# Optimization experiments

Measured on AMD Instinct MI355X. Metric: run time of the kernel, lower is better.

Reference implementation:

```python
import jax, jax.numpy as jnp
import numpy as np

N = 100000          # nodes
F_IN = 500          # num_features
HID = 256           # hidden
C = 40              # out_classes
E = 2302585         # ~ N*ln(N)*ec, doubled (both directions) in spar_samp
ALPHA0 = 0.1        # att[0][0] = alpha*(1-alpha)**0


def setup_inputs() -> dict:
    key = jax.random.key(0)
    ks = jax.random.split(key, 8)
    x = jax.random.normal(ks[0], (N, F_IN), dtype=jnp.float32)
    W1 = jax.random.normal(ks[1], (F_IN, HID), dtype=jnp.float32) * (1.0 / np.sqrt(F_IN))
    b1 = jnp.zeros((HID,), dtype=jnp.float32)
    W2 = jax.random.normal(ks[2], (HID, C), dtype=jnp.float32) * (1.0 / np.sqrt(HID))
    b2 = jnp.zeros((C,), dtype=jnp.float32)
    edge_row = jax.random.randint(ks[3], (E,), 0, N, dtype=jnp.int64) if jax.config.jax_enable_x64 else jax.random.randint(ks[3], (E,), 0, N, dtype=jnp.int32)
    edge_col = jax.random.randint(ks[4], (E,), 0, N, dtype=edge_row.dtype)
    # sampled importance weights: deg^{-1/2}*deg^{-1/2}*(M/num_edgess) -> small positive floats
    edge_val = jax.random.uniform(ks[5], (E,), dtype=jnp.float32, minval=0.001, maxval=0.05)
    return {"x": x, "W1": W1, "b1": b1, "W2": W2, "b2": b2,
            "edge_row": edge_row, "edge_col": edge_col, "edge_val": edge_val}


def reference(x, W1, b1, W2, b2, edge_row, edge_col, edge_val):
    # eval mode: dropout is identity
    h = jax.nn.relu(x @ W1 + b1)          # [N, HID]
    h = h @ W2 + b2                       # [N, C]
    # sparse propagation: out[r] += val * h[c]  (scatter-add SpMM)
    msg = edge_val[:, None] * h[edge_col]            # [E, C] gather
    agg = jax.ops.segment_sum(msg, edge_row, num_segments=N)  # [N, C]
    out = h * ALPHA0 + agg
    return jax.nn.log_softmax(out, axis=1)
```

## Files before the change

### kernel.cpp

```cpp
#include <hip/hip_runtime.h>
#include <hip/hip_bf16.h>


#define N_NODES 100000
#define F_IN    500
#define HID     256
#define C_OUT   40
#define ALPHA0  0.1f
#define H2STRIDE 64

#define RPB     128
#define NBUCK   ((N_NODES + RPB - 1) / RPB)
#define NCH     320
#define SCAN_M  (NBUCK * NCH)
#define SCAN_CHUNK 2048
#define NBS     ((SCAN_M + SCAN_CHUNK - 1) / SCAN_CHUNK)

typedef short short8 __attribute__((ext_vector_type(8)));
typedef float f32x4  __attribute__((ext_vector_type(4)));

__device__ __forceinline__ short f2bf(float f) {
  union { float f; unsigned u; } x; x.f = f;
  unsigned r = x.u + 0x7fffu + ((x.u >> 16) & 1u);
  return (short)(r >> 16);
}
__device__ __forceinline__ float bf2f(short s) {
  union { unsigned u; float f; } x; x.u = ((unsigned)(unsigned short)s) << 16;
  return x.f;
}
__device__ __forceinline__ unsigned cvtpk(float lo, float hi) {
  unsigned r;
  asm("v_cvt_pk_bf16_f32 %0, %1, %2" : "=v"(r) : "v"(lo), "v"(hi));
  return r;
}
__device__ __forceinline__ void lbar() {
  asm volatile("s_waitcnt lgkmcnt(0)" ::: "memory");
  __builtin_amdgcn_s_barrier();
}
__device__ __forceinline__ void gll16(const float* g, const char* l) {
  __builtin_amdgcn_global_load_lds(
      (const __attribute__((address_space(1))) void*)g,
      (__attribute__((address_space(3))) void*)l, 16, 0, 0);
}

__global__ __launch_bounds__(256) void k_pack_weights(
    const float* __restrict__ W1, const float* __restrict__ W2,
    short* __restrict__ W1S, short* __restrict__ W2T)
{
  int i = blockIdx.x * 256 + threadIdx.x;
  if (i < 16*256*32) {
    int kc  = i >> 13;
    int idx = i & 8191;
    int n   = idx >> 5;
    int kk  = idx & 31;
    int k   = kc*32 + kk;
    float v = (k < F_IN) ? W1[k*HID + n] : 0.f;
    W1S[i] = f2bf(v);
  } else {
    int j = i - 16*256*32;
    if (j < 48*256) {
      int n = j >> 8;
      int k = j & 255;
      float v = (n < C_OUT) ? W2[k*C_OUT + n] : 0.f;
      W2T[j] = f2bf(v);
    }
  }
}

__global__ __launch_bounds__(512, 4) void k_fused_mlp(
    const float* __restrict__ x, const float* __restrict__ b1v,
    const float* __restrict__ b2v,
    const short* __restrict__ W1S, const short* __restrict__ W2T,
    short* __restrict__ h2b)
{
  __shared__ __align__(16) char smem[65536];
  short (*Hl)[256] = (short(*)[256])smem;

  const int tid  = threadIdx.x;
  const int w    = tid >> 6;
  const int lane = tid & 63;
  const int lr   = lane & 15;
  const int quad = lane >> 4;
  const int wr   = w >> 2;
  const int wc   = w & 3;
  const int row0 = blockIdx.x * 128;

  const int s_rl0 = (w*2)*8 + (lane>>3);
  const int s_rl1 = (w*2+1)*8 + (lane>>3);
  const int ksw   = ((lane&7) ^ ((lane>>3)&7)) * 4;
  const float* gp0 = x + (size_t)min(row0 + s_rl0, N_NODES-1) * F_IN;
  const float* gp1 = x + (size_t)min(row0 + s_rl1, N_NODES-1) * F_IN;
  const char* l0 = smem + (w*2)*1024;
  const char* l1 = smem + (w*2+1)*1024;

  f32x4 acc[4][4] = {};

  #pragma unroll
  for (int p = 0; p < 2; ++p) {
    int kb = p*32 + ksw;
    const float* a0 = (kb + 4 <= F_IN) ? gp0 + kb : x;
    const float* a1 = (kb + 4 <= F_IN) ? gp1 + kb : x;
    gll16(a0, l0 + p*16384);
    gll16(a1, l1 + p*16384);
  }

  const short* bbase = W1S + (wc*64 + lr)*32 + quad*8;
  const int m2 = lr & 7;

  #pragma unroll
  for (int kc = 0; kc < 16; ++kc) {
    short8 bf4[4];
    #pragma unroll
    for (int t = 0; t < 4; ++t)
      bf4[t] = *(const short8*)(bbase + kc*8192 + t*16*32);
    __builtin_amdgcn_sched_barrier(0);

    if (kc < 14) {
      int kb = (kc+2)*32 + ksw;
      const float* a0 = (kb + 4 <= F_IN) ? gp0 + kb : x;
      const float* a1 = (kb + 4 <= F_IN) ? gp1 + kb : x;
      gll16(a0, l0 + ((kc+2)&3)*16384);
      gll16(a1, l1 + ((kc+2)&3)*16384);
      __builtin_amdgcn_sched_barrier(0);
      asm volatile("s_waitcnt vmcnt(8)" ::: "memory");
    } else if (kc == 14) {
      asm volatile("s_waitcnt vmcnt(6)" ::: "memory");
    } else {
      asm volatile("s_waitcnt vmcnt(4)" ::: "memory");
    }
    __builtin_amdgcn_s_barrier();

    const char* Abase = smem + (kc & 3)*16384;
    short8 af[4];
    #pragma unroll
    for (int t = 0; t < 4; ++t) {
      int rl = wr*64 + t*16 + lr;
      f32x4 u0 = *(const f32x4*)(Abase + rl*128 + (((quad*2  ) ^ m2) << 4));
      f32x4 u1 = *(const f32x4*)(Abase + rl*128 + (((quad*2+1) ^ m2) << 4));
      union { unsigned u[4]; short8 s; } pk;
      pk.u[0] = cvtpk(u0[0], u0[1]);
      pk.u[1] = cvtpk(u0[2], u0[3]);
      pk.u[2] = cvtpk(u1[0], u1[1]);
      pk.u[3] = cvtpk(u1[2], u1[3]);
      af[t] = pk.s;
    }

    #pragma unroll
    for (int rt = 0; rt < 4; ++rt)
      #pragma unroll
      for (int ct = 0; ct < 4; ++ct)
        acc[rt][ct] = __builtin_amdgcn_mfma_f32_16x16x32_bf16(af[rt], bf4[ct], acc[rt][ct], 0, 0, 0);
  }
  lbar();

  #pragma unroll
  for (int ct = 0; ct < 4; ++ct) {
    int col = wc*64 + ct*16 + lr;
    int cg = col >> 3, ci = col & 7;
    float bias = b1v[col];
    #pragma unroll
    for (int rt = 0; rt < 4; ++rt) {
      #pragma unroll
      for (int r = 0; r < 4; ++r) {
        int row = wr*64 + rt*16 + quad*4 + r;
        float v = fmaxf(acc[rt][ct][r] + bias, 0.f);
        Hl[row][((cg ^ (row & 31)) << 3) | ci] = f2bf(v);
      }
    }
  }
  lbar();

  f32x4 acc2[3] = {};
  const int arow = w*16 + lr;
  #pragma unroll
  for (int kc2 = 0; kc2 < 8; ++kc2) {
    int gg = kc2*4 + quad;
    short8 a2 = *(const short8*)&Hl[arow][(gg ^ (arow & 31)) << 3];
    #pragma unroll
    for (int nt = 0; nt < 3; ++nt) {
      short8 b2 = *(const short8*)(W2T + (nt*16 + lr)*256 + kc2*32 + quad*8);
      acc2[nt] = __builtin_amdgcn_mfma_f32_16x16x32_bf16(a2, b2, acc2[nt], 0, 0, 0);
    }
  }

  #pragma unroll
  for (int nt = 0; nt < 3; ++nt) {
    int col = nt*16 + lr;
    float bias = (col < C_OUT) ? b2v[col] : 0.f;
    #pragma unroll
    for (int r = 0; r < 4; ++r) {
      int row = row0 + w*16 + quad*4 + r;
      if (row < N_NODES) {
        float v = (col < C_OUT) ? (acc2[nt][r] + bias) : 0.f;
        h2b[(long)row * H2STRIDE + col] = f2bf(v);
      }
    }
  }
  {
    int col = 48 + lr;
    #pragma unroll
    for (int r = 0; r < 4; ++r) {
      int row = row0 + w*16 + quad*4 + r;
      if (row < N_NODES) h2b[(long)row * H2STRIDE + col] = 0;
    }
  }
}

__global__ __launch_bounds__(256) void k_hist2(
    const int* __restrict__ erow, int* __restrict__ offs, int E, int CH)
{
  __shared__ int h[NBUCK];
  int tid = threadIdx.x, c = blockIdx.x;
  for (int b = tid; b < NBUCK; b += 256) h[b] = 0;
  __syncthreads();
  int e0 = c * CH, e1 = min(E, e0 + CH);
  for (int e = e0 + tid; e < e1; e += 256)
    atomicAdd(&h[erow[e] >> 7], 1);
  __syncthreads();
  for (int b = tid; b < NBUCK; b += 256) offs[b * NCH + c] = h[b];
}

__global__ __launch_bounds__(256) void k_scan1(
    int* __restrict__ offs, int* __restrict__ bsums)
{
  __shared__ int sh[256];
  int tid = threadIdx.x;
  int base = blockIdx.x * SCAN_CHUNK + tid * 8;
  int d[8];
  #pragma unroll
  for (int k = 0; k < 8; ++k)
    d[k] = (base + k < SCAN_M) ? offs[base + k] : 0;
  int s = 0;
  #pragma unroll
  for (int k = 0; k < 8; ++k) s += d[k];
  sh[tid] = s;
  __syncthreads();
  for (int o = 1; o < 256; o <<= 1) {
    int v = (tid >= o) ? sh[tid - o] : 0;
    __syncthreads();
    if (tid >= o) sh[tid] += v;
    __syncthreads();
  }
  int run = sh[tid] - s;
  #pragma unroll
  for (int k = 0; k < 8; ++k) {
    if (base + k < SCAN_M) offs[base + k] = run;
    run += d[k];
  }
  if (tid == 255) bsums[blockIdx.x] = sh[255];
}

__global__ __launch_bounds__(256) void k_scan2(int* __restrict__ bsums) {
  __shared__ int sh[256];
  int tid = threadIdx.x;
  int v = (tid < NBS) ? bsums[tid] : 0;
  sh[tid] = v;
  __syncthreads();
  for (int o = 1; o < 256; o <<= 1) {
    int u = (tid >= o) ? sh[tid - o] : 0;
    __syncthreads();
    if (tid >= o) sh[tid] += u;
    __syncthreads();
  }
  if (tid < NBS) bsums[tid] = sh[tid] - v;
}

__global__ __launch_bounds__(256) void k_scan3(
    int* __restrict__ offs, const int* __restrict__ bsums)
{
  int i = blockIdx.x * 256 + threadIdx.x;
  if (i < SCAN_M) offs[i] += bsums[i >> 11];
}

__global__ __launch_bounds__(256) void k_split(
    const int* __restrict__ erow, const int* __restrict__ ecol,
    const float* __restrict__ eval, const int* __restrict__ offs,
    int2* __restrict__ sorted, int E, int CH)
{
  __shared__ int cur[NBUCK];
  int tid = threadIdx.x, c = blockIdx.x;
  for (int b = tid; b < NBUCK; b += 256) cur[b] = offs[b * NCH + c];
  __syncthreads();
  int e0 = c * CH, e1 = min(E, e0 + CH);
  for (int e = e0 + tid; e < e1; e += 256) {
    int r = erow[e];
    int b = r >> 7;
    int pos = atomicAdd(&cur[b], 1);
    int2 cv;
    cv.x = ecol[e] | ((r & 127) << 17);
    cv.y = __float_as_int(eval[e]);
    sorted[pos] = cv;
  }
}

__global__ __launch_bounds__(256) void k_csr(
    const int* __restrict__ offs, const int2* __restrict__ sorted,
    int2* __restrict__ sorted2, int* __restrict__ row_offs, int E)
{
  __shared__ int hist[RPB];
  __shared__ int scn[RPB];
  int tid = threadIdx.x, b = blockIdx.x;
  int start = offs[b * NCH];
  int end   = (b + 1 < NBUCK) ? offs[(b + 1) * NCH] : E;

  if (tid < RPB) hist[tid] = 0;
  __syncthreads();
  for (int e = start + tid; e < end; e += 256)
    atomicAdd(&hist[((unsigned)sorted[e].x) >> 17], 1);
  __syncthreads();
  if (tid < RPB) scn[tid] = hist[tid];
  __syncthreads();
  for (int o = 1; o < RPB; o <<= 1) {
    int v = (tid >= o && tid < RPB) ? scn[tid - o] : 0;
    __syncthreads();
    if (tid >= o && tid < RPB) scn[tid] += v;
    __syncthreads();
  }
  if (tid < RPB) {
    int excl = scn[tid] - hist[tid];
    int row = b * RPB + tid;
    if (row < N_NODES) row_offs[row] = start + excl;
    hist[tid] = excl;
  }
  __syncthreads();
  for (int e = start + tid; e < end; e += 256) {
    int2 cv = sorted[e];
    int rl = ((unsigned)cv.x) >> 17;
    int pos = start + atomicAdd(&hist[rl], 1);
    sorted2[pos] = cv;
  }
  if (b == 0 && tid == 0) row_offs[N_NODES] = E;
}

__global__ __launch_bounds__(256) void k_spmm_lsm(
    const int* __restrict__ row_offs, const int2* __restrict__ sorted2,
    const short* __restrict__ h2b, float* __restrict__ out)
{
  int row  = blockIdx.x * 4 + (threadIdx.x >> 6);
  int lane = threadIdx.x & 63;
  if (row >= N_NODES) return;

  float acc = ALPHA0 * bf2f(h2b[(long)row * H2STRIDE + lane]);

  int e   = row_offs[row];
  int end = row_offs[row + 1];
  for (; e + 3 < end; e += 4) {
    int2 cv0 = sorted2[e];
    int2 cv1 = sorted2[e + 1];
    int2 cv2 = sorted2[e + 2];
    int2 cv3 = sorted2[e + 3];
    int c0 = cv0.x & 0x1FFFF, c1 = cv1.x & 0x1FFFF;
    int c2 = cv2.x & 0x1FFFF, c3 = cv3.x & 0x1FFFF;
    float g0 = bf2f(h2b[(long)c0 * H2STRIDE + lane]);
    float g1 = bf2f(h2b[(long)c1 * H2STRIDE + lane]);
    float g2 = bf2f(h2b[(long)c2 * H2STRIDE + lane]);
    float g3 = bf2f(h2b[(long)c3 * H2STRIDE + lane]);
    acc += __int_as_float(cv0.y) * g0;
    acc += __int_as_float(cv1.y) * g1;
    acc += __int_as_float(cv2.y) * g2;
    acc += __int_as_float(cv3.y) * g3;
  }
  for (; e < end; ++e) {
    int2 cv = sorted2[e];
    int c0 = cv.x & 0x1FFFF;
    acc += __int_as_float(cv.y) * bf2f(h2b[(long)c0 * H2STRIDE + lane]);
  }

  float m = (lane < C_OUT) ? acc : -INFINITY;
  #pragma unroll
  for (int o = 32; o > 0; o >>= 1) m = fmaxf(m, __shfl_xor(m, o));
  float ev = (lane < C_OUT) ? __expf(acc - m) : 0.f;
  float s = ev;
  #pragma unroll
  for (int o = 32; o > 0; o >>= 1) s += __shfl_xor(s, o);
  if (lane < C_OUT) out[(long)row * C_OUT + lane] = acc - m - __logf(s);
}

extern "C" void kernel_launch(void* const* d_in, const int* in_sizes, int n_in,
                              void* d_out, int out_size, void* d_ws, size_t ws_size,
                              hipStream_t stream) {
  const float* x    = (const float*)d_in[0];
  const float* W1   = (const float*)d_in[1];
  const float* b1   = (const float*)d_in[2];
  const float* W2   = (const float*)d_in[3];
  const float* b2   = (const float*)d_in[4];
  const int*   erow = (const int*)d_in[5];
  const int*   ecol = (const int*)d_in[6];
  const float* eval = (const float*)d_in[7];
  const int E  = in_sizes[5];
  const int CH = (E + NCH - 1) / NCH;

  char* p = (char*)d_ws;
  short* h2b      = (short*)p;  p += (size_t)N_NODES * H2STRIDE * 2;
  short* W1S      = (short*)p;  p += (size_t)16*256*32 * 2;
  short* W2T      = (short*)p;  p += (size_t)48*256 * 2;
  int*   offs     = (int*)p;    p += (size_t)SCAN_M * 4;
  int*   bsums    = (int*)p;    p += 256 * 4;
  int*   row_offs = (int*)p;    p += (size_t)(N_NODES + 4) * 4;
  int2*  sorted   = (int2*)p;   p += (size_t)E * 8;
  int2*  sorted2  = (int2*)p;
  float* out = (float*)d_out;

  k_pack_weights<<<(16*256*32 + 48*256 + 255)/256, 256, 0, stream>>>(W1, W2, W1S, W2T);
  k_fused_mlp<<<(N_NODES + 127)/128, 512, 0, stream>>>(x, b1, b2, W1S, W2T, h2b);
  k_hist2<<<NCH, 256, 0, stream>>>(erow, offs, E, CH);
  k_scan1<<<NBS, 256, 0, stream>>>(offs, bsums);
  k_scan2<<<1, 256, 0, stream>>>(bsums);
  k_scan3<<<(SCAN_M + 255)/256, 256, 0, stream>>>(offs, bsums);
  k_split<<<NCH, 256, 0, stream>>>(erow, ecol, eval, offs, sorted, E, CH);
  k_csr<<<NBUCK, 256, 0, stream>>>(offs, sorted, sorted2, row_offs, E);
  k_spmm_lsm<<<(N_NODES + 3)/4, 256, 0, stream>>>(row_offs, sorted2, h2b, out);
}
```

Measured before the change: 546.8 us.

## Restructure fused MLP so each wave owns 16 rows with register-prefetched A

The first GEMM in the fused MLP now uses 256-thread blocks covering 64 rows, with each wave computing a full 16x256 tile. The x rows are loaded directly from global memory into registers with a one-step prefetch, replacing the LDS staging via global_load_lds and the block barriers. The hidden activations are staged in a per-wave LDS region, so no block-wide sync is needed before the second GEMM. In exchange, every wave now reads all of W1 (four times more B traffic, mostly from cache), holds 16 accumulators per thread, and issues uncoalesced per-row x loads.

```diff
diff --git a/kernel.cpp b/kernel.cpp
--- a/kernel.cpp
+++ b/kernel.cpp
@@ -32,15 +32,6 @@
   unsigned r;
   asm("v_cvt_pk_bf16_f32 %0, %1, %2" : "=v"(r) : "v"(lo), "v"(hi));
   return r;
-}
-__device__ __forceinline__ void lbar() {
-  asm volatile("s_waitcnt lgkmcnt(0)" ::: "memory");
-  __builtin_amdgcn_s_barrier();
-}
-__device__ __forceinline__ void gll16(const float* g, const char* l) {
-  __builtin_amdgcn_global_load_lds(
-      (const __attribute__((address_space(1))) void*)g,
-      (__attribute__((address_space(3))) void*)l, 16, 0, 0);
 }
 
 __global__ __launch_bounds__(256) void k_pack_weights(
@@ -67,115 +58,101 @@
   }
 }
 
-__global__ __launch_bounds__(512, 4) void k_fused_mlp(
+__global__ __launch_bounds__(256, 4) void k_fused_mlp(
     const float* __restrict__ x, const float* __restrict__ b1v,
     const float* __restrict__ b2v,
     const short* __restrict__ W1S, const short* __restrict__ W2T,
     short* __restrict__ h2b)
 {
-  __shared__ __align__(16) char smem[65536];
-  short (*Hl)[256] = (short(*)[256])smem;
+  __shared__ __align__(16) char smem[32768];
 
   const int tid  = threadIdx.x;
   const int w    = tid >> 6;
   const int lane = tid & 63;
   const int lr   = lane & 15;
   const int quad = lane >> 4;
-  const int wr   = w >> 2;
-  const int wc   = w & 3;
-  const int row0 = blockIdx.x * 128;
-
-  const int s_rl0 = (w*2)*8 + (lane>>3);
-  const int s_rl1 = (w*2+1)*8 + (lane>>3);
-  const int ksw   = ((lane&7) ^ ((lane>>3)&7)) * 4;
-  const float* gp0 = x + (size_t)min(row0 + s_rl0, N_NODES-1) * F_IN;
-  const float* gp1 = x + (size_t)min(row0 + s_rl1, N_NODES-1) * F_IN;
-  const char* l0 = smem + (w*2)*1024;
-  const char* l1 = smem + (w*2+1)*1024;
-
-  f32x4 acc[4][4] = {};
-
-  #pragma unroll
-  for (int p = 0; p < 2; ++p) {
-    int kb = p*32 + ksw;
-    const float* a0 = (kb + 4 <= F_IN) ? gp0 + kb : x;
-    const float* a1 = (kb + 4 <= F_IN) ? gp1 + kb : x;
-    gll16(a0, l0 + p*16384);
-    gll16(a1, l1 + p*16384);
-  }
-
-  const short* bbase = W1S + (wc*64 + lr)*32 + quad*8;
-  const int m2 = lr & 7;
-
-  #pragma unroll
+  const int row0 = blockIdx.x * 64;
+
+  const int myrow = row0 + w*16 + lr;
+  const float* ap = x + (size_t)min(myrow, N_NODES - 1) * F_IN;
+
+  f32x4 acc[16] = {};
+
+  float cur[8];
+  {
+    int kb = quad * 8;
+    f32x4 u0 = *(const f32x4*)(ap + kb);
+    f32x4 u1 = *(const f32x4*)(ap + kb + 4);
+    #pragma unroll
+    for (int j = 0; j < 4; ++j) { cur[j] = u0[j]; cur[4+j] = u1[j]; }
+  }
+
+  const short* bb0 = W1S + lr*32 + quad*8;
+
   for (int kc = 0; kc < 16; ++kc) {
-    short8 bf4[4];
-    #pragma unroll
-    for (int t = 0; t < 4; ++t)
-      bf4[t] = *(const short8*)(bbase + kc*8192 + t*16*32);
-    __builtin_amdgcn_sched_barrier(0);
-
-    if (kc < 14) {
-      int kb = (kc+2)*32 + ksw;
-      const float* a0 = (kb + 4 <= F_IN) ? gp0 + kb : x;
-      const float* a1 = (kb + 4 <= F_IN) ? gp1 + kb : x;
-      gll16(a0, l0 + ((kc+2)&3)*16384);
-      gll16(a1, l1 + ((kc+2)&3)*16384);
-      __builtin_amdgcn_sched_barrier(0);
-      asm volatile("s_waitcnt vmcnt(8)" ::: "memory");
-    } else if (kc == 14) {
-      asm volatile("s_waitcnt vmcnt(6)" ::: "memory");
-    } else {
-      asm volatile("s_waitcnt vmcnt(4)" ::: "memory");
-    }
-    __builtin_amdgcn_s_barrier();
-
-    const char* Abase = smem + (kc & 3)*16384;
-    short8 af[4];
-    #pragma unroll
-    for (int t = 0; t < 4; ++t) {
-      int rl = wr*64 + t*16 + lr;
-      f32x4 u0 = *(const f32x4*)(Abase + rl*128 + (((quad*2  ) ^ m2) << 4));
-      f32x4 u1 = *(const f32x4*)(Abase + rl*128 + (((quad*2+1) ^ m2) << 4));
+    float nxt[8];
+    if (kc < 15) {
+      int kb = (kc + 1)*32 + quad*8;
+      if (kb + 8 <= F_IN) {
+        f32x4 u0 = *(const f32x4*)(ap + kb);
+        f32x4 u1 = *(const f32x4*)(ap + kb + 4);
+        #pragma unroll
+        for (int j = 0; j < 4; ++j) { nxt[j] = u0[j]; nxt[4+j] = u1[j]; }
+      } else {
+        #pragma unroll
+        for (int j = 0; j < 8; ++j)
+          nxt[j] = (kb + j < F_IN) ? ap[kb + j] : 0.f;
+      }
+    }
+
+    short8 af;
+    {
       union { unsigned u[4]; short8 s; } pk;
-      pk.u[0] = cvtpk(u0[0], u0[1]);
-      pk.u[1] = cvtpk(u0[2], u0[3]);
-      pk.u[2] = cvtpk(u1[0], u1[1]);
-      pk.u[3] = cvtpk(u1[2], u1[3]);
-      af[t] = pk.s;
-    }
-
-    #pragma unroll
-    for (int rt = 0; rt < 4; ++rt)
+      pk.u[0] = cvtpk(cur[0], cur[1]);
+      pk.u[1] = cvtpk(cur[2], cur[3]);
+      pk.u[2] = cvtpk(cur[4], cur[5]);
+      pk.u[3] = cvtpk(cur[6], cur[7]);
+      af = pk.s;
+    }
+
+    const short* bb = bb0 + kc*8192;
+    #pragma unroll
+    for (int g = 0; g < 4; ++g) {
+      short8 bq[4];
       #pragma unroll
-      for (int ct = 0; ct < 4; ++ct)
-        acc[rt][ct] = __builtin_amdgcn_mfma_f32_16x16x32_bf16(af[rt], bf4[ct], acc[rt][ct], 0, 0, 0);
-  }
-  lbar();
-
-  #pragma unroll
-  for (int ct = 0; ct < 4; ++ct) {
-    int col = wc*64 + ct*16 + lr;
+      for (int t = 0; t < 4; ++t)
+        bq[t] = *(const short8*)(bb + (g*4 + t)*16*32);
+      #pragma unroll
+      for (int t = 0; t < 4; ++t)
+        acc[g*4 + t] = __builtin_amdgcn_mfma_f32_16x16x32_bf16(af, bq[t], acc[g*4 + t], 0, 0, 0);
+    }
+
+    if (kc < 15) {
+      #pragma unroll
+      for (int j = 0; j < 8; ++j) cur[j] = nxt[j];
+    }
+  }
+
+  short (*Hw)[256] = (short(*)[256])(smem + w*8192);
+  #pragma unroll
+  for (int ct = 0; ct < 16; ++ct) {
+    int col = ct*16 + lr;
     int cg = col >> 3, ci = col & 7;
     float bias = b1v[col];
     #pragma unroll
-    for (int rt = 0; rt < 4; ++rt) {
-      #pragma unroll
-      for (int r = 0; r < 4; ++r) {
-        int row = wr*64 + rt*16 + quad*4 + r;
-        float v = fmaxf(acc[rt][ct][r] + bias, 0.f);
-        Hl[row][((cg ^ (row & 31)) << 3) | ci] = f2bf(v);
-      }
-    }
-  }
-  lbar();
+    for (int r = 0; r < 4; ++r) {
+      int row = quad*4 + r;
+      float v = fmaxf(acc[ct][r] + bias, 0.f);
+      Hw[row][((cg ^ row) << 3) | ci] = f2bf(v);
+    }
+  }
 
   f32x4 acc2[3] = {};
-  const int arow = w*16 + lr;
+  const int arow = lr;
   #pragma unroll
   for (int kc2 = 0; kc2 < 8; ++kc2) {
     int gg = kc2*4 + quad;
-    short8 a2 = *(const short8*)&Hl[arow][(gg ^ (arow & 31)) << 3];
+    short8 a2 = *(const short8*)&Hw[arow][(gg ^ arow) << 3];
     #pragma unroll
     for (int nt = 0; nt < 3; ++nt) {
       short8 b2 = *(const short8*)(W2T + (nt*16 + lr)*256 + kc2*32 + quad*8);
@@ -402,7 +379,7 @@
   float* out = (float*)d_out;
 
   k_pack_weights<<<(16*256*32 + 48*256 + 255)/256, 256, 0, stream>>>(W1, W2, W1S, W2T);
-  k_fused_mlp<<<(N_NODES + 127)/128, 512, 0, stream>>>(x, b1, b2, W1S, W2T, h2b);
+  k_fused_mlp<<<(N_NODES + 63)/64, 256, 0, stream>>>(x, b1, b2, W1S, W2T, h2b);
   k_hist2<<<NCH, 256, 0, stream>>>(erow, offs, E, CH);
   k_scan1<<<NBS, 256, 0, stream>>>(offs, bsums);
   k_scan2<<<1, 256, 0, stream>>>(bsums);
```

Result: slower. 601.4 us (+10.0%).

## Fuse CSR build and SpMM into bucket-level kernel with LDS atomic accumulation

Applied to the files above, without the earlier changes.

Drops the per-bucket CSR sort (k_csr) and the per-row SpMM kernel. One block now handles each 128-row bucket: it streams that bucket's edges, gathers h2 rows, and accumulates into a shared-memory [128x40] tile with LDS atomics, then runs log-softmax. This saves a kernel launch and a full read/write pass over the edge array, at the cost of LDS atomic contention and only 782 blocks of parallelism, each with about 2900 edges.

```diff
diff --git a/kernel.cpp b/kernel.cpp
--- a/kernel.cpp
+++ b/kernel.cpp
@@ -293,87 +293,72 @@
   }
 }
 
-__global__ __launch_bounds__(256) void k_csr(
+__global__ __launch_bounds__(256) void k_spmm_bucket(
     const int* __restrict__ offs, const int2* __restrict__ sorted,
-    int2* __restrict__ sorted2, int* __restrict__ row_offs, int E)
-{
-  __shared__ int hist[RPB];
-  __shared__ int scn[RPB];
+    const short* __restrict__ h2b, float* __restrict__ out, int E)
+{
+  __shared__ float accL[RPB][C_OUT];
   int tid = threadIdx.x, b = blockIdx.x;
+  int lane = tid & 63, w = tid >> 6;
   int start = offs[b * NCH];
   int end   = (b + 1 < NBUCK) ? offs[(b + 1) * NCH] : E;
 
-  if (tid < RPB) hist[tid] = 0;
-  __syncthreads();
-  for (int e = start + tid; e < end; e += 256)
-    atomicAdd(&hist[((unsigned)sorted[e].x) >> 17], 1);
-  __syncthreads();
-  if (tid < RPB) scn[tid] = hist[tid];
-  __syncthreads();
-  for (int o = 1; o < RPB; o <<= 1) {
-    int v = (tid >= o && tid < RPB) ? scn[tid - o] : 0;
-    __syncthreads();
-    if (tid >= o && tid < RPB) scn[tid] += v;
-    __syncthreads();
-  }
-  if (tid < RPB) {
-    int excl = scn[tid] - hist[tid];
-    int row = b * RPB + tid;
-    if (row < N_NODES) row_offs[row] = start + excl;
-    hist[tid] = excl;
-  }
-  __syncthreads();
-  for (int e = start + tid; e < end; e += 256) {
-    int2 cv = sorted[e];
-    int rl = ((unsigned)cv.x) >> 17;
-    int pos = start + atomicAdd(&hist[rl], 1);
-    sorted2[pos] = cv;
-  }
-  if (b == 0 && tid == 0) row_offs[N_NODES] = E;
-}
-
-__global__ __launch_bounds__(256) void k_spmm_lsm(
-    const int* __restrict__ row_offs, const int2* __restrict__ sorted2,
-    const short* __restrict__ h2b, float* __restrict__ out)
-{
-  int row  = blockIdx.x * 4 + (threadIdx.x >> 6);
-  int lane = threadIdx.x & 63;
-  if (row >= N_NODES) return;
-
-  float acc = ALPHA0 * bf2f(h2b[(long)row * H2STRIDE + lane]);
-
-  int e   = row_offs[row];
-  int end = row_offs[row + 1];
-  for (; e + 3 < end; e += 4) {
-    int2 cv0 = sorted2[e];
-    int2 cv1 = sorted2[e + 1];
-    int2 cv2 = sorted2[e + 2];
-    int2 cv3 = sorted2[e + 3];
-    int c0 = cv0.x & 0x1FFFF, c1 = cv1.x & 0x1FFFF;
-    int c2 = cv2.x & 0x1FFFF, c3 = cv3.x & 0x1FFFF;
-    float g0 = bf2f(h2b[(long)c0 * H2STRIDE + lane]);
-    float g1 = bf2f(h2b[(long)c1 * H2STRIDE + lane]);
-    float g2 = bf2f(h2b[(long)c2 * H2STRIDE + lane]);
-    float g3 = bf2f(h2b[(long)c3 * H2STRIDE + lane]);
-    acc += __int_as_float(cv0.y) * g0;
-    acc += __int_as_float(cv1.y) * g1;
-    acc += __int_as_float(cv2.y) * g2;
-    acc += __int_as_float(cv3.y) * g3;
-  }
-  for (; e < end; ++e) {
-    int2 cv = sorted2[e];
-    int c0 = cv.x & 0x1FFFF;
-    acc += __int_as_float(cv.y) * bf2f(h2b[(long)c0 * H2STRIDE + lane]);
-  }
-
-  float m = (lane < C_OUT) ? acc : -INFINITY;
-  #pragma unroll
-  for (int o = 32; o > 0; o >>= 1) m = fmaxf(m, __shfl_xor(m, o));
-  float ev = (lane < C_OUT) ? __expf(acc - m) : 0.f;
-  float s = ev;
-  #pragma unroll
-  for (int o = 32; o > 0; o >>= 1) s += __shfl_xor(s, o);
-  if (lane < C_OUT) out[(long)row * C_OUT + lane] = acc - m - __logf(s);
+  for (int i = tid; i < RPB * C_OUT; i += 256) ((float*)accL)[i] = 0.f;
+  __syncthreads();
+
+  for (int base = start + w*64; base < end; base += 256) {
+    int rem = end - base;
+    int2 cv;
+    cv.x = 0; cv.y = 0;
+    if (lane < rem) cv = sorted[base + lane];
+    if (rem >= 64) {
+      for (int i = 0; i < 64; i += 8) {
+        int rl[8]; float vv[8], gg[8];
+        #pragma unroll
+        for (int j = 0; j < 8; ++j) {
+          int cx = __shfl(cv.x, i + j);
+          int vy = __shfl(cv.y, i + j);
+          int c  = cx & 0x1FFFF;
+          rl[j] = ((unsigned)cx) >> 17;
+          vv[j] = __int_as_float(vy);
+          gg[j] = bf2f(h2b[(size_t)c * H2STRIDE + lane]);
+        }
+        if (lane < C_OUT) {
+          #pragma unroll
+          for (int j = 0; j < 8; ++j)
+            atomicAdd(&accL[rl[j]][lane], vv[j] * gg[j]);
+        }
+      }
+    } else {
+      for (int i = 0; i < rem; ++i) {
+        int cx = __shfl(cv.x, i);
+        int vy = __shfl(cv.y, i);
+        int c  = cx & 0x1FFFF;
+        int rl = ((unsigned)cx) >> 17;
+        float g = bf2f(h2b[(size_t)c * H2STRIDE + lane]);
+        if (lane < C_OUT)
+          atomicAdd(&accL[rl][lane], __int_as_float(vy) * g);
+      }
+    }
+  }
+  __syncthreads();
+
+  for (int rr = 0; rr < 32; ++rr) {
+    int r = w*32 + rr;
+    int row = b * RPB + r;
+    if (row >= N_NODES) continue;
+    float a = -INFINITY;
+    if (lane < C_OUT)
+      a = accL[r][lane] + ALPHA0 * bf2f(h2b[(size_t)row * H2STRIDE + lane]);
+    float m = a;
+    #pragma unroll
+    for (int o = 32; o > 0; o >>= 1) m = fmaxf(m, __shfl_xor(m, o));
+    float ev = (lane < C_OUT) ? __expf(a - m) : 0.f;
+    float s = ev;
+    #pragma unroll
+    for (int o = 32; o > 0; o >>= 1) s += __shfl_xor(s, o);
+    if (lane < C_OUT) out[(long)row * C_OUT + lane] = a - m - __logf(s);
+  }
 }
 
 extern "C" void kernel_launch(void* const* d_in, const int* in_sizes, int n_in,
@@ -396,9 +381,7 @@
   short* W2T      = (short*)p;  p += (size_t)48*256 * 2;
   int*   offs     = (int*)p;    p += (size_t)SCAN_M * 4;
   int*   bsums    = (int*)p;    p += 256 * 4;
-  int*   row_offs = (int*)p;    p += (size_t)(N_NODES + 4) * 4;
-  int2*  sorted   = (int2*)p;   p += (size_t)E * 8;
-  int2*  sorted2  = (int2*)p;
+  int2*  sorted   = (int2*)p;
   float* out = (float*)d_out;
 
   k_pack_weights<<<(16*256*32 + 48*256 + 255)/256, 256, 0, stream>>>(W1, W2, W1S, W2T);
@@ -408,6 +391,5 @@
   k_scan2<<<1, 256, 0, stream>>>(bsums);
   k_scan3<<<(SCAN_M + 255)/256, 256, 0, stream>>>(offs, bsums);
   k_split<<<NCH, 256, 0, stream>>>(erow, ecol, eval, offs, sorted, E, CH);
-  k_csr<<<NBUCK, 256, 0, stream>>>(offs, sorted, sorted2, row_offs, E);
-  k_spmm_lsm<<<(N_NODES + 3)/4, 256, 0, stream>>>(row_offs, sorted2, h2b, out);
-}
+  k_spmm_bucket<<<NBUCK, 256, 0, stream>>>(offs, sorted, h2b, out, E);
+}
```

New measurement: 1.160 ms. +112.1%, slower.

## Replace two-pass bucketed CSR build with direct per-row global atomic histogram and scatter

Applied to the files above, without the earlier changes.

The CSR construction no longer uses a two-level scheme (per-chunk bucket histograms in LDS, a large scan, a bucket split, then a per-bucket local sort). It now counts edges per row with global atomics, scans the N+1 row counts, and scatters edges straight into CSR order with global atomic cursors. The row-count array is zeroed inside the weight-pack kernel. This removes one full pass over the edge array and the intermediate sorted buffer, along with the large scan. In exchange it takes on heavy global atomic contention across roughly 2.3M edges and produces a nondeterministic order of edges within each row, which changes summation order.

```diff
diff --git a/kernel.cpp b/kernel.cpp
--- a/kernel.cpp
+++ b/kernel.cpp
@@ -9,12 +9,8 @@
 #define ALPHA0  0.1f
 #define H2STRIDE 64
 
-#define RPB     128
-#define NBUCK   ((N_NODES + RPB - 1) / RPB)
-#define NCH     320
-#define SCAN_M  (NBUCK * NCH)
 #define SCAN_CHUNK 2048
-#define NBS     ((SCAN_M + SCAN_CHUNK - 1) / SCAN_CHUNK)
+#define NBS_R   ((N_NODES + SCAN_CHUNK - 1) / SCAN_CHUNK)
 
 typedef short short8 __attribute__((ext_vector_type(8)));
 typedef float f32x4  __attribute__((ext_vector_type(4)));
@@ -45,7 +41,8 @@
 
 __global__ __launch_bounds__(256) void k_pack_weights(
     const float* __restrict__ W1, const float* __restrict__ W2,
-    short* __restrict__ W1S, short* __restrict__ W2T)
+    short* __restrict__ W1S, short* __restrict__ W2T,
+    int* __restrict__ rcnt)
 {
   int i = blockIdx.x * 256 + threadIdx.x;
   if (i < 16*256*32) {
@@ -56,14 +53,15 @@
     int k   = kc*32 + kk;
     float v = (k < F_IN) ? W1[k*HID + n] : 0.f;
     W1S[i] = f2bf(v);
+  } else if (i < 16*256*32 + 48*256) {
+    int j = i - 16*256*32;
+    int n = j >> 8;
+    int k = j & 255;
+    float v = (n < C_OUT) ? W2[k*C_OUT + n] : 0.f;
+    W2T[j] = f2bf(v);
   } else {
-    int j = i - 16*256*32;
-    if (j < 48*256) {
-      int n = j >> 8;
-      int k = j & 255;
-      float v = (n < C_OUT) ? W2[k*C_OUT + n] : 0.f;
-      W2T[j] = f2bf(v);
-    }
+    int j = i - (16*256*32 + 48*256);
+    if (j <= N_NODES) rcnt[j] = 0;
   }
 }
 
@@ -206,18 +204,13 @@
   }
 }
 
-__global__ __launch_bounds__(256) void k_hist2(
-    const int* __restrict__ erow, int* __restrict__ offs, int E, int CH)
-{
-  __shared__ int h[NBUCK];
-  int tid = threadIdx.x, c = blockIdx.x;
-  for (int b = tid; b < NBUCK; b += 256) h[b] = 0;
-  __syncthreads();
-  int e0 = c * CH, e1 = min(E, e0 + CH);
-  for (int e = e0 + tid; e < e1; e += 256)
-    atomicAdd(&h[erow[e] >> 7], 1);
-  __syncthreads();
-  for (int b = tid; b < NBUCK; b += 256) offs[b * NCH + c] = h[b];
+__global__ __launch_bounds__(256) void k_hist_rows(
+    const int* __restrict__ erow, int* __restrict__ rcnt, int E)
+{
+  int i = blockIdx.x * 256 + threadIdx.x;
+  int stride = gridDim.x * 256;
+  for (int e = i; e < E; e += stride)
+    atomicAdd(&rcnt[erow[e]], 1);
 }
 
 __global__ __launch_bounds__(256) void k_scan1(
@@ -229,7 +222,7 @@
   int d[8];
   #pragma unroll
   for (int k = 0; k < 8; ++k)
-    d[k] = (base + k < SCAN_M) ? offs[base + k] : 0;
+    d[k] = (base + k < N_NODES) ? offs[base + k] : 0;
   int s = 0;
   #pragma unroll
   for (int k = 0; k < 8; ++k) s += d[k];
@@ -244,7 +237,7 @@
   int run = sh[tid] - s;
   #pragma unroll
   for (int k = 0; k < 8; ++k) {
-    if (base + k < SCAN_M) offs[base + k] = run;
+    if (base + k < N_NODES) offs[base + k] = run;
     run += d[k];
   }
   if (tid == 255) bsums[blockIdx.x] = sh[255];
@@ -253,7 +246,7 @@
 __global__ __launch_bounds__(256) void k_scan2(int* __restrict__ bsums) {
   __shared__ int sh[256];
   int tid = threadIdx.x;
-  int v = (tid < NBS) ? bsums[tid] : 0;
+  int v = (tid < NBS_R) ? bsums[tid] : 0;
   sh[tid] = v;
   __syncthreads();
   for (int o = 1; o < 256; o <<= 1) {
@@ -262,74 +255,37 @@
     if (tid >= o) sh[tid] += u;
     __syncthreads();
   }
-  if (tid < NBS) bsums[tid] = sh[tid] - v;
+  if (tid < NBS_R) bsums[tid] = sh[tid] - v;
 }
 
 __global__ __launch_bounds__(256) void k_scan3(
-    int* __restrict__ offs, const int* __restrict__ bsums)
+    int* __restrict__ offs, const int* __restrict__ bsums,
+    int* __restrict__ cur, int E)
 {
   int i = blockIdx.x * 256 + threadIdx.x;
-  if (i < SCAN_M) offs[i] += bsums[i >> 11];
-}
-
-__global__ __launch_bounds__(256) void k_split(
+  if (i < N_NODES) {
+    int v = offs[i] + bsums[i >> 11];
+    offs[i] = v;
+    cur[i]  = v;
+  }
+  if (i == 0) offs[N_NODES] = E;
+}
+
+__global__ __launch_bounds__(256) void k_scatter(
     const int* __restrict__ erow, const int* __restrict__ ecol,
-    const float* __restrict__ eval, const int* __restrict__ offs,
-    int2* __restrict__ sorted, int E, int CH)
-{
-  __shared__ int cur[NBUCK];
-  int tid = threadIdx.x, c = blockIdx.x;
-  for (int b = tid; b < NBUCK; b += 256) cur[b] = offs[b * NCH + c];
-  __syncthreads();
-  int e0 = c * CH, e1 = min(E, e0 + CH);
-  for (int e = e0 + tid; e < e1; e += 256) {
+    const float* __restrict__ eval, int* __restrict__ cur,
+    int2* __restrict__ sorted2, int E)
+{
+  int i = blockIdx.x * 256 + threadIdx.x;
+  int stride = gridDim.x * 256;
+  for (int e = i; e < E; e += stride) {
     int r = erow[e];
-    int b = r >> 7;
-    int pos = atomicAdd(&cur[b], 1);
+    int pos = atomicAdd(&cur[r], 1);
     int2 cv;
-    cv.x = ecol[e] | ((r & 127) << 17);
+    cv.x = ecol[e];
     cv.y = __float_as_int(eval[e]);
-    sorted[pos] = cv;
-  }
-}
-
-__global__ __launch_bounds__(256) void k_csr(
-    const int* __restrict__ offs, const int2* __restrict__ sorted,
-    int2* __restrict__ sorted2, int* __restrict__ row_offs, int E)
-{
-  __shared__ int hist[RPB];
-  __shared__ int scn[RPB];
-  int tid = threadIdx.x, b = blockIdx.x;
-  int start = offs[b * NCH];
-  int end   = (b + 1 < NBUCK) ? offs[(b + 1) * NCH] : E;
-
-  if (tid < RPB) hist[tid] = 0;
-  __syncthreads();
-  for (int e = start + tid; e < end; e += 256)
-    atomicAdd(&hist[((unsigned)sorted[e].x) >> 17], 1);
-  __syncthreads();
-  if (tid < RPB) scn[tid] = hist[tid];
-  __syncthreads();
-  for (int o = 1; o < RPB; o <<= 1) {
-    int v = (tid >= o && tid < RPB) ? scn[tid - o] : 0;
-    __syncthreads();
-    if (tid >= o && tid < RPB) scn[tid] += v;
-    __syncthreads();
-  }
-  if (tid < RPB) {
-    int excl = scn[tid] - hist[tid];
-    int row = b * RPB + tid;
-    if (row < N_NODES) row_offs[row] = start + excl;
-    hist[tid] = excl;
-  }
-  __syncthreads();
-  for (int e = start + tid; e < end; e += 256) {
-    int2 cv = sorted[e];
-    int rl = ((unsigned)cv.x) >> 17;
-    int pos = start + atomicAdd(&hist[rl], 1);
     sorted2[pos] = cv;
   }
-  if (b == 0 && tid == 0) row_offs[N_NODES] = E;
 }
 
 __global__ __launch_bounds__(256) void k_spmm_lsm(
@@ -349,12 +305,10 @@
     int2 cv1 = sorted2[e + 1];
     int2 cv2 = sorted2[e + 2];
     int2 cv3 = sorted2[e + 3];
-    int c0 = cv0.x & 0x1FFFF, c1 = cv1.x & 0x1FFFF;
-    int c2 = cv2.x & 0x1FFFF, c3 = cv3.x & 0x1FFFF;
-    float g0 = bf2f(h2b[(long)c0 * H2STRIDE + lane]);
-    float g1 = bf2f(h2b[(long)c1 * H2STRIDE + lane]);
-    float g2 = bf2f(h2b[(long)c2 * H2STRIDE + lane]);
-    float g3 = bf2f(h2b[(long)c3 * H2STRIDE + lane]);
+    float g0 = bf2f(h2b[(size_t)cv0.x * H2STRIDE + lane]);
+    float g1 = bf2f(h2b[(size_t)cv1.x * H2STRIDE + lane]);
+    float g2 = bf2f(h2b[(size_t)cv2.x * H2STRIDE + lane]);
+    float g3 = bf2f(h2b[(size_t)cv3.x * H2STRIDE + lane]);
     acc += __int_as_float(cv0.y) * g0;
     acc += __int_as_float(cv1.y) * g1;
     acc += __int_as_float(cv2.y) * g2;
@@ -362,8 +316,7 @@
   }
   for (; e < end; ++e) {
     int2 cv = sorted2[e];
-    int c0 = cv.x & 0x1FFFF;
-    acc += __int_as_float(cv.y) * bf2f(h2b[(long)c0 * H2STRIDE + lane]);
+    acc += __int_as_float(cv.y) * bf2f(h2b[(size_t)cv.x * H2STRIDE + lane]);
   }
 
   float m = (lane < C_OUT) ? acc : -INFINITY;
@@ -388,26 +341,24 @@
   const int*   ecol = (const int*)d_in[6];
   const float* eval = (const float*)d_in[7];
   const int E  = in_sizes[5];
-  const int CH = (E + NCH - 1) / NCH;
 
   char* p = (char*)d_ws;
   short* h2b      = (short*)p;  p += (size_t)N_NODES * H2STRIDE * 2;
   short* W1S      = (short*)p;  p += (size_t)16*256*32 * 2;
   short* W2T      = (short*)p;  p += (size_t)48*256 * 2;
-  int*   offs     = (int*)p;    p += (size_t)SCAN_M * 4;
+  int*   row_offs = (int*)p;    p += (size_t)(N_NODES + 4) * 4;
+  int*   cursor   = (int*)p;    p += (size_t)(N_NODES + 4) * 4;
   int*   bsums    = (int*)p;    p += 256 * 4;
-  int*   row_offs = (int*)p;    p += (size_t)(N_NODES + 4) * 4;
-  int2*  sorted   = (int2*)p;   p += (size_t)E * 8;
   int2*  sorted2  = (int2*)p;
   float* out = (float*)d_out;
 
-  k_pack_weights<<<(16*256*32 + 48*256 + 255)/256, 256, 0, stream>>>(W1, W2, W1S, W2T);
+  const int pack_work = 16*256*32 + 48*256 + N_NODES + 1;
+  k_pack_weights<<<(pack_work + 255)/256, 256, 0, stream>>>(W1, W2, W1S, W2T, row_offs);
   k_fused_mlp<<<(N_NODES + 127)/128, 512, 0, stream>>>(x, b1, b2, W1S, W2T, h2b);
-  k_hist2<<<NCH, 256, 0, stream>>>(erow, offs, E, CH);
-  k_scan1<<<NBS, 256, 0, stream>>>(offs, bsums);
+  k_hist_rows<<<2048, 256, 0, stream>>>(erow, row_offs, E);
+  k_scan1<<<NBS_R, 256, 0, stream>>>(row_offs, bsums);
   k_scan2<<<1, 256, 0, stream>>>(bsums);
-  k_scan3<<<(SCAN_M + 255)/256, 256, 0, stream>>>(offs, bsums);
-  k_split<<<NCH, 256, 0, stream>>>(erow, ecol, eval, offs, sorted, E, CH);
-  k_csr<<<NBUCK, 256, 0, stream>>>(offs, sorted, sorted2, row_offs, E);
+  k_scan3<<<(N_NODES + 255)/256, 256, 0, stream>>>(row_offs, bsums, cursor, E);
+  k_scatter<<<2048, 256, 0, stream>>>(erow, ecol, eval, cursor, sorted2, E);
   k_spmm_lsm<<<(N_NODES + 3)/4, 256, 0, stream>>>(row_offs, sorted2, h2b, out);
 }
```

Measured after the change: 730.3 us. 1.34x slower.
